# Kernel optimization log

Hardware: AMD Instinct MI355X
Metric: run time of the kernel (lower is better)

## Reference

```python
import jax, jax.numpy as jnp
import numpy as np

B, T, N = 64, 128, 64   # batch, win_size, input_size (= node_num)
H, E, K, CS = 64, 128, 7, 8  # hidden_size, embed_size, kernel_size, control_size
NEG_SLOPE = 0.2


def _p(key, shape, scale=0.05):
    return scale * jax.random.normal(key, shape, dtype=jnp.float32)


def setup_inputs() -> dict:
    key = jax.random.key(0)
    ks = jax.random.split(key, 32)
    inp = {
        "x": jax.random.normal(ks[0], (B, T, N), dtype=jnp.float32),
        "y": jax.random.normal(ks[1], (B, T, CS), dtype=jnp.float32),
        # Conv1d(N -> N, kernel K)
        "conv_w": _p(ks[2], (N, N, K)),
        "conv_b": _p(ks[3], (N,)),
        # rnn_enc GRU: input N -> hidden H
        "We_ih": _p(ks[4], (3 * H, N)), "We_hh": _p(ks[5], (3 * H, H)),
        "be_ih": _p(ks[6], (3 * H,)), "be_hh": _p(ks[7], (3 * H,)),
        # MP_GAT linears
        "Ww": _p(ks[8], (E, 2 * T)), "bw": _p(ks[9], (E,)),
        "Wa": _p(ks[10], (1, E)), "ba": _p(ks[11], (1,)),
        # encoder GRU: input H+N -> H
        "Wm_ih": _p(ks[12], (3 * H, H + N)), "Wm_hh": _p(ks[13], (3 * H, H)),
        "bm_ih": _p(ks[14], (3 * H,)), "bm_hh": _p(ks[15], (3 * H,)),
        # rnn_dec GRU: input H -> H
        "Wd_ih": _p(ks[16], (3 * H, H)), "Wd_hh": _p(ks[17], (3 * H, H)),
        "bd_ih": _p(ks[18], (3 * H,)), "bd_hh": _p(ks[19], (3 * H,)),
        # fc_dec: H -> N
        "W_dec": _p(ks[20], (N, H)), "b_dec": _p(ks[21], (N,)),
        # fc_pred: Linear(H,N), ReLU, Linear(N,N)
        "W_p1": _p(ks[22], (N, H)), "b_p1": _p(ks[23], (N,)),
        "W_p2": _p(ks[24], (N, N)), "b_p2": _p(ks[25], (N,)),
    }
    return inp


def gru_seq(x_seq, Wih, Whh, bih, bhh):
    """torch nn.GRU (batch_first, h0=0). x_seq: [B,T,in] -> [B,T,H]."""
    gi = jnp.einsum('bti,gi->btg', x_seq, Wih) + bih  # [B,T,3H] (precompute input proj)
    h0 = jnp.zeros((x_seq.shape[0], Whh.shape[1]), x_seq.dtype)

    def step(h, gi_t):
        gh = h @ Whh.T + bhh
        i_r, i_z, i_n = jnp.split(gi_t, 3, axis=-1)
        h_r, h_z, h_n = jnp.split(gh, 3, axis=-1)
        r = jax.nn.sigmoid(i_r + h_r)
        z = jax.nn.sigmoid(i_z + h_z)
        n = jnp.tanh(i_n + r * h_n)
        h_new = (1.0 - z) * n + z * h
        return h_new, h_new

    _, hs = jax.lax.scan(step, h0, jnp.swapaxes(gi, 0, 1))
    return jnp.swapaxes(hs, 0, 1)


def _forward(x, y, conv_w, conv_b, We_ih, We_hh, be_ih, be_hh, Ww, bw, Wa, ba,
             Wm_ih, Wm_hh, bm_ih, bm_hh, Wd_ih, Wd_hh, bd_ih, bd_hh,
             W_dec, b_dec, W_p1, b_p1, W_p2, b_p2):
    # ---- CNN: pad 'same' + Conv1d + SELU. x: [B,T,N] -> channels first [B,N,T]
    pad = (K - 1) // 2
    xc = jnp.swapaxes(x, 1, 2)
    c = jax.lax.conv_general_dilated(xc, conv_w, (1,), [(pad, pad)],
                                     dimension_numbers=('NCH', 'OIH', 'NCH'))
    c = jax.nn.selu(c + conv_b[None, :, None])  # [B,N,T]
    c_btn = jnp.swapaxes(c, 1, 2)               # [B,T,N]

    # ---- rnn_enc GRU over time
    h_out = gru_seq(c_btn, We_ih, We_hh, be_ih, be_hh)  # [B,T,H]

    # ---- MP_GAT on c (v: [B, node, seq] = [B,N,T])
    v = c
    vi = jnp.broadcast_to(v[:, :, None, :], (B, N, N, T))
    vj = jnp.broadcast_to(v[:, None, :, :], (B, N, N, T))
    v_cat = jnp.concatenate([vi, vj], axis=-1)          # [B,N,N,2T]
    x_w = jax.nn.leaky_relu(jnp.einsum('bijt,et->bije', v_cat, Ww) + bw, NEG_SLOPE)
    e = (jnp.einsum('bije,oe->bijo', x_w, Wa) + ba)[..., 0]  # [B,N,N]
    attention = jax.nn.softmax(e, axis=2)
    # dropout is identity in eval mode
    h_mp = jax.nn.sigmoid(jnp.einsum('bij,bjt->bit', attention, v))  # [B,N,T]
    h_mp = jnp.swapaxes(h_mp, 1, 2)                      # [B,T,N]

    # ---- encoder / decoder GRUs (dropout = identity in eval)
    h_cat = jnp.concatenate([h_out, h_mp], axis=2)       # [B,T,H+N]
    h_enc = gru_seq(h_cat, Wm_ih, Wm_hh, bm_ih, bm_hh)
    h_dec = gru_seq(h_enc, Wd_ih, Wd_hh, bd_ih, bd_hh)

    recon = h_dec @ W_dec.T + b_dec                      # [B,T,N]
    p = jax.nn.relu(h_dec[:, 0, :] @ W_p1.T + b_p1)
    pred = p @ W_p2.T + b_p2                             # [B,N]
    return recon, pred


def reference(x, y, conv_w, conv_b, We_ih, We_hh, be_ih, be_hh, Ww, bw, Wa, ba,
              Wm_ih, Wm_hh, bm_ih, bm_hh, Wd_ih, Wd_hh, bd_ih, bd_hh,
              W_dec, b_dec, W_p1, b_p1, W_p2, b_p2):
    return _forward(x, y, conv_w, conv_b, We_ih, We_hh, be_ih, be_hh, Ww, bw, Wa, ba,
                    Wm_ih, Wm_hh, bm_ih, bm_hh, Wd_ih, Wd_hh, bd_ih, bd_hh,
                    W_dec, b_dec, W_p1, b_p1, W_p2, b_p2)
```

## Files before the change

kernel.cpp:

```cpp
#include <hip/hip_runtime.h>
#include <math.h>

#define BB 64
#define TT 128
#define NN 64
#define HH 64
#define EE 128
#define KK 7
#define GG 192

typedef _Float16 half2_t __attribute__((ext_vector_type(2)));

__device__ __forceinline__ float sigmoidf_(float x){ return 1.f/(1.f+expf(-x)); }
__device__ __forceinline__ float fsig_(float x){
  return __builtin_amdgcn_rcpf(1.f + __builtin_amdgcn_exp2f(-1.44269504f * x));
}
__device__ __forceinline__ float ftanh_(float x){
  return fmaf(-2.f, __builtin_amdgcn_rcpf(1.f + __builtin_amdgcn_exp2f(2.88539008f * x)), 1.f);
}

#define PIPE_BARRIER() asm volatile("s_waitcnt lgkmcnt(0)\ns_barrier" ::: "memory")

__device__ __forceinline__ void loadrow_(float* d, const float* src){
  const float4* p = (const float4*)src;
  #pragma unroll
  for (int i = 0; i < 16; ++i) {
    float4 v = p[i];
    d[4*i] = v.x; d[4*i+1] = v.y; d[4*i+2] = v.z; d[4*i+3] = v.w;
  }
}
__device__ __forceinline__ void loadroww_(half2_t* d, const float* src){
  const float4* p = (const float4*)src;
  #pragma unroll
  for (int i = 0; i < 16; ++i) {
    float4 v = p[i];
    d[2*i]   = half2_t{(_Float16)v.x, (_Float16)v.y};
    d[2*i+1] = half2_t{(_Float16)v.z, (_Float16)v.w};
  }
}
__device__ __forceinline__ void load_h16_(const _Float16* hs, half2_t* hp){
  const float4* s4 = (const float4*)hs;
  #pragma unroll
  for (int j = 0; j < 8; ++j) {
    float4 v = s4[j];
    const half2_t* q = (const half2_t*)&v;
    hp[4*j] = q[0]; hp[4*j+1] = q[1]; hp[4*j+2] = q[2]; hp[4*j+3] = q[3];
  }
}
__device__ __forceinline__ void mvdot3_(const half2_t* hp, const half2_t* w0,
                                        const half2_t* w1, const half2_t* w2,
                                        float& a0, float& a1, float& a2){
  #pragma unroll
  for (int i = 0; i < 32; ++i) {
    a0 = __builtin_amdgcn_fdot2(hp[i], w0[i], a0, false);
    a1 = __builtin_amdgcn_fdot2(hp[i], w1[i], a1, false);
    a2 = __builtin_amdgcn_fdot2(hp[i], w2[i], a2, false);
  }
}

__global__ void conv_selu_kernel(const float* __restrict__ x, const float* __restrict__ w,
                                 const float* __restrict__ bias,
                                 float* __restrict__ c_nt, float* __restrict__ c_btn) {
  const int og = blockIdx.x, b = blockIdx.y, t = threadIdx.x;
  const int o0 = og * 8;
  __shared__ __align__(16) float xs[NN][TT + 1];
  __shared__ __align__(16) float ws[NN * KK][8];
  for (int idx = t; idx < TT * NN; idx += 128) {
    int tt = idx >> 6, nn = idx & 63;
    xs[nn][tt] = x[(size_t)(b * TT + tt) * NN + nn];
  }
  for (int idx = t; idx < NN * KK * 8; idx += 128) {
    int oo = idx & 7, ik = idx >> 3;
    ws[ik][oo] = w[(size_t)(o0 + oo) * (NN * KK) + ik];
  }
  __syncthreads();
  float acc[8];
  #pragma unroll
  for (int oo = 0; oo < 8; ++oo) acc[oo] = bias[o0 + oo];
  for (int i = 0; i < NN; ++i) {
    #pragma unroll
    for (int k = 0; k < KK; ++k) {
      int tt = t + k - 3;
      if (tt >= 0 && tt < TT) {
        float xv = xs[i][tt];
        const float* wp = &ws[i * KK + k][0];
        float4 w0 = *(const float4*)wp;
        float4 w1 = *(const float4*)(wp + 4);
        acc[0] += xv * w0.x; acc[1] += xv * w0.y; acc[2] += xv * w0.z; acc[3] += xv * w0.w;
        acc[4] += xv * w1.x; acc[5] += xv * w1.y; acc[6] += xv * w1.z; acc[7] += xv * w1.w;
      }
    }
  }
  const float alpha = 1.6732632423543772f, scale = 1.0507009873554805f;
  #pragma unroll
  for (int oo = 0; oo < 8; ++oo) {
    float a = acc[oo];
    float r = a > 0.f ? scale * a : scale * alpha * expm1f(a);
    int o = o0 + oo;
    c_nt[((size_t)b * NN + o) * TT + t] = r;
    c_btn[((size_t)b * TT + t) * NN + o] = r;
  }
}

__global__ void s12_kernel(const float* __restrict__ c_nt, const float* __restrict__ Ww,
                           float* __restrict__ s1, float* __restrict__ s2) {
  const int m0 = blockIdx.x * 16, col = threadIdx.x;
  __shared__ __align__(16) float ins[16][TT];
  for (int idx = col; idx < 16 * TT; idx += 128) {
    int r = idx >> 7, k = idx & 127;
    ins[r][k] = c_nt[(size_t)(m0 + r) * TT + k];
  }
  __syncthreads();
  const float* w1 = Ww + (size_t)col * (2 * TT);
  const float* w2 = w1 + TT;
  float acc1[16], acc2[16];
  #pragma unroll
  for (int r = 0; r < 16; ++r) { acc1[r] = 0.f; acc2[r] = 0.f; }
  #pragma unroll 2
  for (int k = 0; k < TT; k += 4) {
    float4 wv1 = *(const float4*)(w1 + k);
    float4 wv2 = *(const float4*)(w2 + k);
    #pragma unroll
    for (int r = 0; r < 16; ++r) {
      float4 iv = *(const float4*)&ins[r][k];
      acc1[r] += iv.x * wv1.x + iv.y * wv1.y + iv.z * wv1.z + iv.w * wv1.w;
      acc2[r] += iv.x * wv2.x + iv.y * wv2.y + iv.z * wv2.z + iv.w * wv2.w;
    }
  }
  #pragma unroll
  for (int r = 0; r < 16; ++r) {
    s1[(size_t)(m0 + r) * EE + col] = acc1[r];
    s2[(size_t)(m0 + r) * EE + col] = acc2[r];
  }
}

__global__ void gat_kernel(const float* __restrict__ s1, const float* __restrict__ s2,
                           const float* __restrict__ bw, const float* __restrict__ Wa,
                           const float* __restrict__ ba, const float* __restrict__ c_nt,
                           float* __restrict__ hmp) {
  const int i = blockIdx.x, b = blockIdx.y, tid = threadIdx.x;
  __shared__ float s2s[NN][EE + 1];
  __shared__ float s1b[EE], was[EE], att[NN];
  for (int idx = tid; idx < NN * EE; idx += 128) {
    int r = idx >> 7, e = idx & 127;
    s2s[r][e] = s2[((size_t)b * NN + r) * EE + e];
  }
  s1b[tid] = s1[((size_t)b * NN + i) * EE + tid] + bw[tid];
  was[tid] = Wa[tid];
  __syncthreads();
  if (tid < NN) {
    float acc = 0.f;
    #pragma unroll 8
    for (int e = 0; e < EE; ++e) {
      float wv = s1b[e] + s2s[tid][e];
      wv = wv > 0.f ? wv : 0.2f * wv;
      acc += was[e] * wv;
    }
    float ej = acc + ba[0];
    float mx = ej;
    for (int off = 32; off >= 1; off >>= 1) mx = fmaxf(mx, __shfl_xor(mx, off));
    float ex = expf(ej - mx);
    float sm = ex;
    for (int off = 32; off >= 1; off >>= 1) sm += __shfl_xor(sm, off);
    att[tid] = ex / sm;
  }
  __syncthreads();
  float acc = 0.f;
  #pragma unroll 8
  for (int j = 0; j < NN; ++j) acc += att[j] * c_nt[((size_t)b * NN + j) * TT + tid];
  hmp[((size_t)b * TT + tid) * NN + i] = sigmoidf_(acc);
}

__global__ __launch_bounds__(512, 1)
void fused_chain8(const float* __restrict__ c_btn, const float* __restrict__ hmp,
                  const float* __restrict__ We_ih, const float* __restrict__ be_ih,
                  const float* __restrict__ We_hh, const float* __restrict__ be_hh,
                  const float* __restrict__ Wm_ih, const float* __restrict__ bm_ih,
                  const float* __restrict__ Wm_hh, const float* __restrict__ bm_hh,
                  const float* __restrict__ Wd_ih, const float* __restrict__ bd_ih,
                  const float* __restrict__ Wd_hh, const float* __restrict__ bd_hh,
                  const float* __restrict__ W_dec, const float* __restrict__ b_dec,
                  const float* __restrict__ W_p1, const float* __restrict__ b_p1,
                  const float* __restrict__ W_p2, const float* __restrict__ b_p2,
                  float* __restrict__ recon, float* __restrict__ pred) {
  const int b = blockIdx.x, tid = threadIdx.x, wid = tid >> 6, g = tid & 63;
  __shared__ __align__(16) _Float16 cbuf[2][HH], mbuf[2][HH];
  __shared__ __align__(16) _Float16 h1h[2][HH], h2h[2][HH], h3h[2][HH];
  __shared__ __align__(16) float h3f[2][HH];
  __shared__ __align__(16) float q1[2][GG], q2a[2][GG], q2b[2][GG], q3[2][GG];
  __shared__ __align__(16) float h0s[HH], ps[HH];

  half2_t wa[32], wb[32], wc[32];
  float wdec[64];
  float b0 = 0.f, b1 = 0.f, b2 = 0.f;
  float e0 = 0.f, e1 = 0.f, e2 = 0.f;
  if (wid == 0) {
    loadroww_(wa, We_hh + (size_t)g * HH);
    loadroww_(wb, We_hh + (size_t)(g + 64) * HH);
    loadroww_(wc, We_hh + (size_t)(g + 128) * HH);
    b0 = be_hh[g]; b1 = be_hh[64 + g]; b2 = be_hh[128 + g];
  } else if (wid == 1) {
    loadroww_(wa, Wm_hh + (size_t)g * HH);
    loadroww_(wb, Wm_hh + (size_t)(g + 64) * HH);
    loadroww_(wc, Wm_hh + (size_t)(g + 128) * HH);
    b0 = bm_hh[g]; b1 = bm_hh[64 + g]; b2 = bm_hh[128 + g];
  } else if (wid == 2) {
    loadroww_(wa, Wd_hh + (size_t)g * HH);
    loadroww_(wb, Wd_hh + (size_t)(g + 64) * HH);
    loadroww_(wc, Wd_hh + (size_t)(g + 128) * HH);
    b0 = bd_hh[g]; b1 = bd_hh[64 + g]; b2 = bd_hh[128 + g];
    e0 = bd_ih[g]; e1 = bd_ih[64 + g]; e2 = bd_ih[128 + g];
  } else if (wid == 3) {
    loadrow_(wdec, W_dec + (size_t)g * HH);
    b0 = b_dec[g];
  } else if (wid == 4) {
    loadroww_(wa, Wm_ih + (size_t)g * 128);
    loadroww_(wb, Wm_ih + (size_t)(g + 64) * 128);
    loadroww_(wc, Wm_ih + (size_t)(g + 128) * 128);
  } else if (wid == 5) {
    loadroww_(wa, Wd_ih + (size_t)g * HH);
    loadroww_(wb, Wd_ih + (size_t)(g + 64) * HH);
    loadroww_(wc, Wd_ih + (size_t)(g + 128) * HH);
  } else if (wid == 6) {
    loadroww_(wa, We_ih + (size_t)g * HH);
    loadroww_(wb, We_ih + (size_t)(g + 64) * HH);
    loadroww_(wc, We_ih + (size_t)(g + 128) * HH);
    b0 = be_ih[g]; b1 = be_ih[64 + g]; b2 = be_ih[128 + g];
  } else {
    loadroww_(wa, Wm_ih + (size_t)g * 128 + 64);
    loadroww_(wb, Wm_ih + (size_t)(g + 64) * 128 + 64);
    loadroww_(wc, Wm_ih + (size_t)(g + 128) * 128 + 64);
    b0 = bm_ih[g]; b1 = bm_ih[64 + g]; b2 = bm_ih[128 + g];
  }

  if (wid == 0) {
    h1h[0][g] = (_Float16)0.f; h1h[1][g] = (_Float16)0.f;
    h2h[0][g] = (_Float16)0.f; h2h[1][g] = (_Float16)0.f;
    h3h[0][g] = (_Float16)0.f; h3h[1][g] = (_Float16)0.f;
  }
  const float* cb = c_btn + (size_t)b * TT * NN + g;
  const float* hm = hmp   + (size_t)b * TT * NN + g;
  float pf0 = 0.f, pf1 = 0.f;
  if (wid == 6) {
    cbuf[0][g] = (_Float16)cb[0]; cbuf[1][g] = (_Float16)cb[NN];
    pf0 = cb[2 * NN]; pf1 = cb[3 * NN];
  }
  if (wid == 7) {
    mbuf[0][g] = (_Float16)hm[0]; mbuf[1][g] = (_Float16)hm[NN];
    pf0 = hm[2 * NN]; pf1 = hm[3 * NN];
  }
  if (wid <= 2) __builtin_amdgcn_s_setprio(1);
  __syncthreads();

  float hown = 0.f;
  for (int ph = 0; ph < TT + 6; ++ph) {
    const int pw = ph & 1, pr = pw ^ 1;
    if (wid == 6) {
      int t = ph;
      if (t < TT) {
        half2_t hp[32]; load_h16_(&cbuf[pw][0], hp);
        if (t + 2 < TT) cbuf[pw][g] = (_Float16)(pw ? pf1 : pf0);
        float a0 = b0, a1 = b1, a2 = b2;
        if (t + 4 < TT) { float nv = cb[(size_t)(t + 4) * NN]; if (pw) pf1 = nv; else pf0 = nv; }
        mvdot3_(hp, wa, wb, wc, a0, a1, a2);
        q1[pw][g] = a0; q1[pw][64 + g] = a1; q1[pw][128 + g] = a2;
      }
    } else if (wid == 0) {
      int t = ph - 1;
      if (t >= 0 && t < TT) {
        half2_t hp[32]; load_h16_(&h1h[pr][0], hp);
        float a0 = b0, a1 = b1, a2 = b2;
        mvdot3_(hp, wa, wb, wc, a0, a1, a2);
        float r = fsig_(q1[pr][g] + a0), z = fsig_(q1[pr][64 + g] + a1);
        float n = ftanh_(q1[pr][128 + g] + r * a2);
        hown = fmaf(z, hown - n, n);
        h1h[pw][g] = (_Float16)hown;
      }
    } else if (wid == 4) {
      int t = ph - 2;
      if (t >= 0 && t < TT) {
        half2_t hp[32]; load_h16_(&h1h[pr][0], hp);
        float a0 = 0.f, a1 = 0.f, a2 = 0.f;
        mvdot3_(hp, wa, wb, wc, a0, a1, a2);
        q2a[pw][g] = a0; q2a[pw][64 + g] = a1; q2a[pw][128 + g] = a2;
      }
    } else if (wid == 7) {
      int t = ph - 2;
      if (t >= 0 && t < TT) {
        half2_t hp[32]; load_h16_(&mbuf[pw][0], hp);
        if (t + 2 < TT) mbuf[pw][g] = (_Float16)(pw ? pf1 : pf0);
        float a0 = b0, a1 = b1, a2 = b2;
        if (t + 4 < TT) { float nv = hm[(size_t)(t + 4) * NN]; if (pw) pf1 = nv; else pf0 = nv; }
        mvdot3_(hp, wa, wb, wc, a0, a1, a2);
        q2b[pw][g] = a0; q2b[pw][64 + g] = a1; q2b[pw][128 + g] = a2;
      }
    } else if (wid == 1) {
      int t = ph - 3;
      if (t >= 0 && t < TT) {
        half2_t hp[32]; load_h16_(&h2h[pr][0], hp);
        float a0 = b0, a1 = b1, a2 = b2;
        mvdot3_(hp, wa, wb, wc, a0, a1, a2);
        float gr = q2a[pr][g] + q2b[pr][g];
        float gz = q2a[pr][64 + g] + q2b[pr][64 + g];
        float gn = q2a[pr][128 + g] + q2b[pr][128 + g];
        float r = fsig_(gr + a0), z = fsig_(gz + a1), n = ftanh_(gn + r * a2);
        hown = fmaf(z, hown - n, n);
        h2h[pw][g] = (_Float16)hown;
      }
    } else if (wid == 5) {
      int t = ph - 4;
      if (t >= 0 && t < TT) {
        half2_t hp[32]; load_h16_(&h2h[pr][0], hp);
        float a0 = 0.f, a1 = 0.f, a2 = 0.f;
        mvdot3_(hp, wa, wb, wc, a0, a1, a2);
        q3[pw][g] = a0; q3[pw][64 + g] = a1; q3[pw][128 + g] = a2;
      }
    } else if (wid == 2) {
      int t = ph - 5;
      if (t >= 0 && t < TT) {
        half2_t hp[32]; load_h16_(&h3h[pr][0], hp);
        float a0 = b0, a1 = b1, a2 = b2;
        mvdot3_(hp, wa, wb, wc, a0, a1, a2);
        float r = fsig_(q3[pr][g] + e0 + a0), z = fsig_(q3[pr][64 + g] + e1 + a1);
        float n = ftanh_(q3[pr][128 + g] + e2 + r * a2);
        hown = fmaf(z, hown - n, n);
        h3h[pw][g] = (_Float16)hown;
        h3f[pw][g] = hown;
        if (t == 0) h0s[g] = hown;
      }
    } else {
      int t = ph - 6;
      if (t >= 0) {
        const float4* h4 = (const float4*)&h3f[pr][0];
        float a0 = b0, a1 = 0.f;
        #pragma unroll
        for (int i = 0; i < 8; ++i) {
          float4 hv = h4[2 * i], hw = h4[2 * i + 1];
          a0 = fmaf(hv.x, wdec[8*i],   fmaf(hv.y, wdec[8*i+1], fmaf(hv.z, wdec[8*i+2], fmaf(hv.w, wdec[8*i+3], a0))));
          a1 = fmaf(hw.x, wdec[8*i+4], fmaf(hw.y, wdec[8*i+5], fmaf(hw.z, wdec[8*i+6], fmaf(hw.w, wdec[8*i+7], a1))));
        }
        recon[((size_t)b * TT + t) * NN + g] = a0 + a1;
      }
    }
    PIPE_BARRIER();
  }

  if (wid == 0) {
    float w1r[64]; loadrow_(w1r, W_p1 + (size_t)g * HH);
    const float4* h4 = (const float4*)&h0s[0];
    float a = b_p1[g];
    #pragma unroll
    for (int i = 0; i < 16; ++i) {
      float4 hv = h4[i];
      a = fmaf(hv.x, w1r[4*i], fmaf(hv.y, w1r[4*i+1], fmaf(hv.z, w1r[4*i+2], fmaf(hv.w, w1r[4*i+3], a))));
    }
    ps[g] = fmaxf(a, 0.f);
    asm volatile("s_waitcnt lgkmcnt(0)" ::: "memory");
    float w2r[64]; loadrow_(w2r, W_p2 + (size_t)g * HH);
    const float4* p4 = (const float4*)&ps[0];
    float c2 = b_p2[g];
    #pragma unroll
    for (int i = 0; i < 16; ++i) {
      float4 pv = p4[i];
      c2 = fmaf(pv.x, w2r[4*i], fmaf(pv.y, w2r[4*i+1], fmaf(pv.z, w2r[4*i+2], fmaf(pv.w, w2r[4*i+3], c2))));
    }
    pred[(size_t)b * NN + g] = c2;
  }
}

extern "C" void kernel_launch(void* const* d_in, const int* in_sizes, int n_in,
                              void* d_out, int out_size, void* d_ws, size_t ws_size,
                              hipStream_t stream) {
  const float* x      = (const float*)d_in[0];
  const float* conv_w = (const float*)d_in[2];
  const float* conv_b = (const float*)d_in[3];
  const float* We_ih  = (const float*)d_in[4];
  const float* We_hh  = (const float*)d_in[5];
  const float* be_ih  = (const float*)d_in[6];
  const float* be_hh  = (const float*)d_in[7];
  const float* Ww     = (const float*)d_in[8];
  const float* bw     = (const float*)d_in[9];
  const float* Wa     = (const float*)d_in[10];
  const float* ba     = (const float*)d_in[11];
  const float* Wm_ih  = (const float*)d_in[12];
  const float* Wm_hh  = (const float*)d_in[13];
  const float* bm_ih  = (const float*)d_in[14];
  const float* bm_hh  = (const float*)d_in[15];
  const float* Wd_ih  = (const float*)d_in[16];
  const float* Wd_hh  = (const float*)d_in[17];
  const float* bd_ih  = (const float*)d_in[18];
  const float* bd_hh  = (const float*)d_in[19];
  const float* W_dec  = (const float*)d_in[20];
  const float* b_dec  = (const float*)d_in[21];
  const float* W_p1   = (const float*)d_in[22];
  const float* b_p1   = (const float*)d_in[23];
  const float* W_p2   = (const float*)d_in[24];
  const float* b_p2   = (const float*)d_in[25];
  float* out = (float*)d_out;

  float* wsf   = (float*)d_ws;
  float* c_nt  = wsf;
  float* c_btn = c_nt  + 524288;
  float* s1    = c_btn + 524288;
  float* s2    = s1    + 524288;
  float* hmp   = s2    + 524288;

  conv_selu_kernel<<<dim3(8, BB), 128, 0, stream>>>(x, conv_w, conv_b, c_nt, c_btn);
  s12_kernel<<<BB * NN / 16, 128, 0, stream>>>(c_nt, Ww, s1, s2);
  gat_kernel<<<dim3(NN, BB), 128, 0, stream>>>(s1, s2, bw, Wa, ba, c_nt, hmp);
  fused_chain8<<<BB, 512, 0, stream>>>(c_btn, hmp,
                                       We_ih, be_ih, We_hh, be_hh,
                                       Wm_ih, bm_ih, Wm_hh, bm_hh,
                                       Wd_ih, bd_ih, Wd_hh, bd_hh,
                                       W_dec, b_dec, W_p1, b_p1, W_p2, b_p2,
                                       out, out + BB * TT * NN);
}
```

Baseline: 206.0 us.

## Restructure GRU chain pipeline to 4 waves and batch GAT rows per block

The fused recurrent chain drops from 8 to 4 waves per block. Each wave now computes both the input and hidden projections of one GRU layer, so the pipeline depth shrinks from 6 stages to 4 with fewer barrier phases and fewer shared-memory staging buffers. The GAT kernel processes 16 attention rows per block with c_nt cached in shared memory, which cuts redundant s2 and c_nt reloads, and it uses exp2 in the softmax. The cost is more work per wave on the serial critical path (six dot-product accumulators instead of three) and higher register pressure.

```diff
diff --git a/kernel.cpp b/kernel.cpp
--- a/kernel.cpp
+++ b/kernel.cpp
@@ -20,6 +20,7 @@
 }
 
 #define PIPE_BARRIER() asm volatile("s_waitcnt lgkmcnt(0)\ns_barrier" ::: "memory")
+#define LGKM0() asm volatile("s_waitcnt lgkmcnt(0)" ::: "memory")
 
 __device__ __forceinline__ void loadrow_(float* d, const float* src){
   const float4* p = (const float4*)src;
@@ -36,25 +37,6 @@
     float4 v = p[i];
     d[2*i]   = half2_t{(_Float16)v.x, (_Float16)v.y};
     d[2*i+1] = half2_t{(_Float16)v.z, (_Float16)v.w};
-  }
-}
-__device__ __forceinline__ void load_h16_(const _Float16* hs, half2_t* hp){
-  const float4* s4 = (const float4*)hs;
-  #pragma unroll
-  for (int j = 0; j < 8; ++j) {
-    float4 v = s4[j];
-    const half2_t* q = (const half2_t*)&v;
-    hp[4*j] = q[0]; hp[4*j+1] = q[1]; hp[4*j+2] = q[2]; hp[4*j+3] = q[3];
-  }
-}
-__device__ __forceinline__ void mvdot3_(const half2_t* hp, const half2_t* w0,
-                                        const half2_t* w1, const half2_t* w2,
-                                        float& a0, float& a1, float& a2){
-  #pragma unroll
-  for (int i = 0; i < 32; ++i) {
-    a0 = __builtin_amdgcn_fdot2(hp[i], w0[i], a0, false);
-    a1 = __builtin_amdgcn_fdot2(hp[i], w1[i], a1, false);
-    a2 = __builtin_amdgcn_fdot2(hp[i], w2[i], a2, false);
   }
 }
 
@@ -138,41 +120,58 @@
                            const float* __restrict__ bw, const float* __restrict__ Wa,
                            const float* __restrict__ ba, const float* __restrict__ c_nt,
                            float* __restrict__ hmp) {
-  const int i = blockIdx.x, b = blockIdx.y, tid = threadIdx.x;
+  const int it = blockIdx.x, b = blockIdx.y, tid = threadIdx.x;
+  const int i0 = it * 16;
   __shared__ float s2s[NN][EE + 1];
-  __shared__ float s1b[EE], was[EE], att[NN];
-  for (int idx = tid; idx < NN * EE; idx += 128) {
+  __shared__ float s1b[16][EE];
+  __shared__ float cs[NN][TT + 1];
+  __shared__ float was[EE];
+  __shared__ float att[16][NN];
+  for (int idx = tid; idx < NN * EE; idx += 256) {
+    int j = idx >> 7, e = idx & 127;
+    s2s[j][e] = s2[((size_t)b * NN + j) * EE + e] + bw[e];
+  }
+  for (int idx = tid; idx < 16 * EE; idx += 256) {
     int r = idx >> 7, e = idx & 127;
-    s2s[r][e] = s2[((size_t)b * NN + r) * EE + e];
-  }
-  s1b[tid] = s1[((size_t)b * NN + i) * EE + tid] + bw[tid];
-  was[tid] = Wa[tid];
+    s1b[r][e] = s1[((size_t)b * NN + i0 + r) * EE + e];
+  }
+  for (int idx = tid; idx < NN * TT; idx += 256) {
+    int j = idx >> 7, t = idx & 127;
+    cs[j][t] = c_nt[((size_t)b * NN + j) * TT + t];
+  }
+  if (tid < EE) was[tid] = Wa[tid];
   __syncthreads();
-  if (tid < NN) {
+  const int wv = tid >> 6, j = tid & 63;
+  #pragma unroll
+  for (int pass = 0; pass < 4; ++pass) {
+    const int il = pass * 4 + wv;
     float acc = 0.f;
     #pragma unroll 8
     for (int e = 0; e < EE; ++e) {
-      float wv = s1b[e] + s2s[tid][e];
-      wv = wv > 0.f ? wv : 0.2f * wv;
-      acc += was[e] * wv;
+      float v = s1b[il][e] + s2s[j][e];
+      v = v > 0.f ? v : 0.2f * v;
+      acc += was[e] * v;
     }
     float ej = acc + ba[0];
     float mx = ej;
     for (int off = 32; off >= 1; off >>= 1) mx = fmaxf(mx, __shfl_xor(mx, off));
-    float ex = expf(ej - mx);
+    float ex = __builtin_amdgcn_exp2f(1.44269504f * (ej - mx));
     float sm = ex;
     for (int off = 32; off >= 1; off >>= 1) sm += __shfl_xor(sm, off);
-    att[tid] = ex / sm;
+    att[il][j] = ex / sm;
   }
   __syncthreads();
-  float acc = 0.f;
-  #pragma unroll 8
-  for (int j = 0; j < NN; ++j) acc += att[j] * c_nt[((size_t)b * NN + j) * TT + tid];
-  hmp[((size_t)b * TT + tid) * NN + i] = sigmoidf_(acc);
-}
-
-__global__ __launch_bounds__(512, 1)
-void fused_chain8(const float* __restrict__ c_btn, const float* __restrict__ hmp,
+  for (int o = tid; o < 16 * TT; o += 256) {
+    int il = o >> 7, t = o & 127;
+    float acc = 0.f;
+    #pragma unroll 8
+    for (int jj = 0; jj < NN; ++jj) acc += att[il][jj] * cs[jj][t];
+    hmp[((size_t)b * TT + t) * NN + i0 + il] = sigmoidf_(acc);
+  }
+}
+
+__global__ __launch_bounds__(256, 1)
+void fused_chain4(const float* __restrict__ c_btn, const float* __restrict__ hmp,
                   const float* __restrict__ We_ih, const float* __restrict__ be_ih,
                   const float* __restrict__ We_hh, const float* __restrict__ be_hh,
                   const float* __restrict__ Wm_ih, const float* __restrict__ bm_ih,
@@ -184,168 +183,191 @@
                   const float* __restrict__ W_p2, const float* __restrict__ b_p2,
                   float* __restrict__ recon, float* __restrict__ pred) {
   const int b = blockIdx.x, tid = threadIdx.x, wid = tid >> 6, g = tid & 63;
-  __shared__ __align__(16) _Float16 cbuf[2][HH], mbuf[2][HH];
-  __shared__ __align__(16) _Float16 h1h[2][HH], h2h[2][HH], h3h[2][HH];
-  __shared__ __align__(16) float h3f[2][HH];
-  __shared__ __align__(16) float q1[2][GG], q2a[2][GG], q2b[2][GG], q3[2][GG];
+  __shared__ __align__(16) _Float16 cbuf[HH], mbuf[HH], h3h[HH];
+  __shared__ __align__(16) _Float16 h1h[2][HH], h2h[2][HH];
+  __shared__ __align__(16) float q2[2][GG], h3f[2][HH];
   __shared__ __align__(16) float h0s[HH], ps[HH];
 
-  half2_t wa[32], wb[32], wc[32];
+  half2_t wxa[32], wxb[32], wxc[32];
+  half2_t wya[32], wyb[32], wyc[32];
   float wdec[64];
-  float b0 = 0.f, b1 = 0.f, b2 = 0.f;
-  float e0 = 0.f, e1 = 0.f, e2 = 0.f;
+  float b0 = 0.f, b1 = 0.f, b2 = 0.f, e0 = 0.f, e1 = 0.f, e2 = 0.f, bdc = 0.f;
   if (wid == 0) {
-    loadroww_(wa, We_hh + (size_t)g * HH);
-    loadroww_(wb, We_hh + (size_t)(g + 64) * HH);
-    loadroww_(wc, We_hh + (size_t)(g + 128) * HH);
-    b0 = be_hh[g]; b1 = be_hh[64 + g]; b2 = be_hh[128 + g];
+    loadroww_(wxa, We_ih + (size_t)g * HH);
+    loadroww_(wxb, We_ih + (size_t)(g + 64) * HH);
+    loadroww_(wxc, We_ih + (size_t)(g + 128) * HH);
+    loadroww_(wya, We_hh + (size_t)g * HH);
+    loadroww_(wyb, We_hh + (size_t)(g + 64) * HH);
+    loadroww_(wyc, We_hh + (size_t)(g + 128) * HH);
+    b0 = be_ih[g]; b1 = be_ih[64 + g]; b2 = be_ih[128 + g];
+    e0 = be_hh[g]; e1 = be_hh[64 + g]; e2 = be_hh[128 + g];
   } else if (wid == 1) {
-    loadroww_(wa, Wm_hh + (size_t)g * HH);
-    loadroww_(wb, Wm_hh + (size_t)(g + 64) * HH);
-    loadroww_(wc, Wm_hh + (size_t)(g + 128) * HH);
+    loadroww_(wxa, Wm_ih + (size_t)g * 128);
+    loadroww_(wxb, Wm_ih + (size_t)(g + 64) * 128);
+    loadroww_(wxc, Wm_ih + (size_t)(g + 128) * 128);
+    loadroww_(wya, Wm_ih + (size_t)g * 128 + 64);
+    loadroww_(wyb, Wm_ih + (size_t)(g + 64) * 128 + 64);
+    loadroww_(wyc, Wm_ih + (size_t)(g + 128) * 128 + 64);
+    b0 = bm_ih[g]; b1 = bm_ih[64 + g]; b2 = bm_ih[128 + g];
+  } else if (wid == 2) {
+    loadroww_(wxa, Wm_hh + (size_t)g * HH);
+    loadroww_(wxb, Wm_hh + (size_t)(g + 64) * HH);
+    loadroww_(wxc, Wm_hh + (size_t)(g + 128) * HH);
+    loadrow_(wdec, W_dec + (size_t)g * HH);
     b0 = bm_hh[g]; b1 = bm_hh[64 + g]; b2 = bm_hh[128 + g];
-  } else if (wid == 2) {
-    loadroww_(wa, Wd_hh + (size_t)g * HH);
-    loadroww_(wb, Wd_hh + (size_t)(g + 64) * HH);
-    loadroww_(wc, Wd_hh + (size_t)(g + 128) * HH);
-    b0 = bd_hh[g]; b1 = bd_hh[64 + g]; b2 = bd_hh[128 + g];
-    e0 = bd_ih[g]; e1 = bd_ih[64 + g]; e2 = bd_ih[128 + g];
-  } else if (wid == 3) {
-    loadrow_(wdec, W_dec + (size_t)g * HH);
-    b0 = b_dec[g];
-  } else if (wid == 4) {
-    loadroww_(wa, Wm_ih + (size_t)g * 128);
-    loadroww_(wb, Wm_ih + (size_t)(g + 64) * 128);
-    loadroww_(wc, Wm_ih + (size_t)(g + 128) * 128);
-  } else if (wid == 5) {
-    loadroww_(wa, Wd_ih + (size_t)g * HH);
-    loadroww_(wb, Wd_ih + (size_t)(g + 64) * HH);
-    loadroww_(wc, Wd_ih + (size_t)(g + 128) * HH);
-  } else if (wid == 6) {
-    loadroww_(wa, We_ih + (size_t)g * HH);
-    loadroww_(wb, We_ih + (size_t)(g + 64) * HH);
-    loadroww_(wc, We_ih + (size_t)(g + 128) * HH);
-    b0 = be_ih[g]; b1 = be_ih[64 + g]; b2 = be_ih[128 + g];
+    bdc = b_dec[g];
   } else {
-    loadroww_(wa, Wm_ih + (size_t)g * 128 + 64);
-    loadroww_(wb, Wm_ih + (size_t)(g + 64) * 128 + 64);
-    loadroww_(wc, Wm_ih + (size_t)(g + 128) * 128 + 64);
-    b0 = bm_ih[g]; b1 = bm_ih[64 + g]; b2 = bm_ih[128 + g];
-  }
-
+    loadroww_(wxa, Wd_ih + (size_t)g * HH);
+    loadroww_(wxb, Wd_ih + (size_t)(g + 64) * HH);
+    loadroww_(wxc, Wd_ih + (size_t)(g + 128) * HH);
+    loadroww_(wya, Wd_hh + (size_t)g * HH);
+    loadroww_(wyb, Wd_hh + (size_t)(g + 64) * HH);
+    loadroww_(wyc, Wd_hh + (size_t)(g + 128) * HH);
+    b0 = bd_ih[g]; b1 = bd_ih[64 + g]; b2 = bd_ih[128 + g];
+    e0 = bd_hh[g]; e1 = bd_hh[64 + g]; e2 = bd_hh[128 + g];
+  }
   if (wid == 0) {
     h1h[0][g] = (_Float16)0.f; h1h[1][g] = (_Float16)0.f;
     h2h[0][g] = (_Float16)0.f; h2h[1][g] = (_Float16)0.f;
-    h3h[0][g] = (_Float16)0.f; h3h[1][g] = (_Float16)0.f;
+    h3h[g]    = (_Float16)0.f;
   }
   const float* cb = c_btn + (size_t)b * TT * NN + g;
   const float* hm = hmp   + (size_t)b * TT * NN + g;
-  float pf0 = 0.f, pf1 = 0.f;
-  if (wid == 6) {
-    cbuf[0][g] = (_Float16)cb[0]; cbuf[1][g] = (_Float16)cb[NN];
-    pf0 = cb[2 * NN]; pf1 = cb[3 * NN];
-  }
-  if (wid == 7) {
-    mbuf[0][g] = (_Float16)hm[0]; mbuf[1][g] = (_Float16)hm[NN];
-    pf0 = hm[2 * NN]; pf1 = hm[3 * NN];
-  }
-  if (wid <= 2) __builtin_amdgcn_s_setprio(1);
+  float cc = 0.f, cn = 0.f;
+  if (wid == 0) { cc = cb[0]; cn = cb[NN]; }
+  if (wid == 1) { cc = hm[0]; cn = hm[NN]; }
+  float hown = 0.f;
   __syncthreads();
 
-  float hown = 0.f;
-  for (int ph = 0; ph < TT + 6; ++ph) {
-    const int pw = ph & 1, pr = pw ^ 1;
-    if (wid == 6) {
-      int t = ph;
+  for (int p = 0; p < TT + 4; ++p) {
+    const int pw = p & 1, pr = pw ^ 1;
+    if (wid == 0) {
+      int t = p;
       if (t < TT) {
-        half2_t hp[32]; load_h16_(&cbuf[pw][0], hp);
-        if (t + 2 < TT) cbuf[pw][g] = (_Float16)(pw ? pf1 : pf0);
-        float a0 = b0, a1 = b1, a2 = b2;
-        if (t + 4 < TT) { float nv = cb[(size_t)(t + 4) * NN]; if (pw) pf1 = nv; else pf0 = nv; }
-        mvdot3_(hp, wa, wb, wc, a0, a1, a2);
-        q1[pw][g] = a0; q1[pw][64 + g] = a1; q1[pw][128 + g] = a2;
-      }
-    } else if (wid == 0) {
-      int t = ph - 1;
-      if (t >= 0 && t < TT) {
-        half2_t hp[32]; load_h16_(&h1h[pr][0], hp);
-        float a0 = b0, a1 = b1, a2 = b2;
-        mvdot3_(hp, wa, wb, wc, a0, a1, a2);
-        float r = fsig_(q1[pr][g] + a0), z = fsig_(q1[pr][64 + g] + a1);
-        float n = ftanh_(q1[pr][128 + g] + r * a2);
+        cbuf[g] = (_Float16)cc;
+        float cl = 0.f;
+        if (t + 2 < TT) cl = cb[(size_t)(t + 2) * NN];
+        LGKM0();
+        float a0 = b0, a1 = b1, a2 = b2, r0 = e0, r1 = e1, r2 = e2;
+        const float4* c4 = (const float4*)&cbuf[0];
+        const float4* h4 = (const float4*)&h1h[pr][0];
+        #pragma unroll
+        for (int ch = 0; ch < 8; ++ch) {
+          float4 cv = c4[ch], hv = h4[ch];
+          const half2_t* cq = (const half2_t*)&cv;
+          const half2_t* hq = (const half2_t*)&hv;
+          #pragma unroll
+          for (int k = 0; k < 4; ++k) {
+            int i = 4 * ch + k;
+            a0 = __builtin_amdgcn_fdot2(cq[k], wxa[i], a0, false);
+            a1 = __builtin_amdgcn_fdot2(cq[k], wxb[i], a1, false);
+            a2 = __builtin_amdgcn_fdot2(cq[k], wxc[i], a2, false);
+            r0 = __builtin_amdgcn_fdot2(hq[k], wya[i], r0, false);
+            r1 = __builtin_amdgcn_fdot2(hq[k], wyb[i], r1, false);
+            r2 = __builtin_amdgcn_fdot2(hq[k], wyc[i], r2, false);
+          }
+        }
+        float r = fsig_(a0 + r0), z = fsig_(a1 + r1), n = ftanh_(a2 + r * r2);
         hown = fmaf(z, hown - n, n);
         h1h[pw][g] = (_Float16)hown;
-      }
-    } else if (wid == 4) {
-      int t = ph - 2;
+        cc = cn; cn = cl;
+      }
+    } else if (wid == 1) {
+      int t = p - 1;
       if (t >= 0 && t < TT) {
-        half2_t hp[32]; load_h16_(&h1h[pr][0], hp);
-        float a0 = 0.f, a1 = 0.f, a2 = 0.f;
-        mvdot3_(hp, wa, wb, wc, a0, a1, a2);
-        q2a[pw][g] = a0; q2a[pw][64 + g] = a1; q2a[pw][128 + g] = a2;
-      }
-    } else if (wid == 7) {
-      int t = ph - 2;
+        mbuf[g] = (_Float16)cc;
+        float cl = 0.f;
+        if (t + 2 < TT) cl = hm[(size_t)(t + 2) * NN];
+        LGKM0();
+        float a0 = b0, a1 = b1, a2 = b2, r0 = 0.f, r1 = 0.f, r2 = 0.f;
+        const float4* h4 = (const float4*)&h1h[pr][0];
+        const float4* m4 = (const float4*)&mbuf[0];
+        #pragma unroll
+        for (int ch = 0; ch < 8; ++ch) {
+          float4 hv = h4[ch], mv = m4[ch];
+          const half2_t* hq = (const half2_t*)&hv;
+          const half2_t* mq = (const half2_t*)&mv;
+          #pragma unroll
+          for (int k = 0; k < 4; ++k) {
+            int i = 4 * ch + k;
+            a0 = __builtin_amdgcn_fdot2(hq[k], wxa[i], a0, false);
+            a1 = __builtin_amdgcn_fdot2(hq[k], wxb[i], a1, false);
+            a2 = __builtin_amdgcn_fdot2(hq[k], wxc[i], a2, false);
+            r0 = __builtin_amdgcn_fdot2(mq[k], wya[i], r0, false);
+            r1 = __builtin_amdgcn_fdot2(mq[k], wyb[i], r1, false);
+            r2 = __builtin_amdgcn_fdot2(mq[k], wyc[i], r2, false);
+          }
+        }
+        q2[pw][g] = a0 + r0; q2[pw][64 + g] = a1 + r1; q2[pw][128 + g] = a2 + r2;
+        cc = cn; cn = cl;
+      }
+    } else if (wid == 2) {
+      int t = p - 2;
       if (t >= 0 && t < TT) {
-        half2_t hp[32]; load_h16_(&mbuf[pw][0], hp);
-        if (t + 2 < TT) mbuf[pw][g] = (_Float16)(pw ? pf1 : pf0);
         float a0 = b0, a1 = b1, a2 = b2;
-        if (t + 4 < TT) { float nv = hm[(size_t)(t + 4) * NN]; if (pw) pf1 = nv; else pf0 = nv; }
-        mvdot3_(hp, wa, wb, wc, a0, a1, a2);
-        q2b[pw][g] = a0; q2b[pw][64 + g] = a1; q2b[pw][128 + g] = a2;
-      }
-    } else if (wid == 1) {
-      int t = ph - 3;
-      if (t >= 0 && t < TT) {
-        half2_t hp[32]; load_h16_(&h2h[pr][0], hp);
-        float a0 = b0, a1 = b1, a2 = b2;
-        mvdot3_(hp, wa, wb, wc, a0, a1, a2);
-        float gr = q2a[pr][g] + q2b[pr][g];
-        float gz = q2a[pr][64 + g] + q2b[pr][64 + g];
-        float gn = q2a[pr][128 + g] + q2b[pr][128 + g];
-        float r = fsig_(gr + a0), z = fsig_(gz + a1), n = ftanh_(gn + r * a2);
+        const float4* h4 = (const float4*)&h2h[pr][0];
+        #pragma unroll
+        for (int ch = 0; ch < 8; ++ch) {
+          float4 hv = h4[ch];
+          const half2_t* hq = (const half2_t*)&hv;
+          #pragma unroll
+          for (int k = 0; k < 4; ++k) {
+            int i = 4 * ch + k;
+            a0 = __builtin_amdgcn_fdot2(hq[k], wxa[i], a0, false);
+            a1 = __builtin_amdgcn_fdot2(hq[k], wxb[i], a1, false);
+            a2 = __builtin_amdgcn_fdot2(hq[k], wxc[i], a2, false);
+          }
+        }
+        float r = fsig_(q2[pr][g] + a0), z = fsig_(q2[pr][64 + g] + a1);
+        float n = ftanh_(q2[pr][128 + g] + r * a2);
         hown = fmaf(z, hown - n, n);
         h2h[pw][g] = (_Float16)hown;
       }
-    } else if (wid == 5) {
-      int t = ph - 4;
-      if (t >= 0 && t < TT) {
-        half2_t hp[32]; load_h16_(&h2h[pr][0], hp);
-        float a0 = 0.f, a1 = 0.f, a2 = 0.f;
-        mvdot3_(hp, wa, wb, wc, a0, a1, a2);
-        q3[pw][g] = a0; q3[pw][64 + g] = a1; q3[pw][128 + g] = a2;
-      }
-    } else if (wid == 2) {
-      int t = ph - 5;
-      if (t >= 0 && t < TT) {
-        half2_t hp[32]; load_h16_(&h3h[pr][0], hp);
-        float a0 = b0, a1 = b1, a2 = b2;
-        mvdot3_(hp, wa, wb, wc, a0, a1, a2);
-        float r = fsig_(q3[pr][g] + e0 + a0), z = fsig_(q3[pr][64 + g] + e1 + a1);
-        float n = ftanh_(q3[pr][128 + g] + e2 + r * a2);
-        hown = fmaf(z, hown - n, n);
-        h3h[pw][g] = (_Float16)hown;
-        h3f[pw][g] = hown;
-        if (t == 0) h0s[g] = hown;
-      }
-    } else {
-      int t = ph - 6;
-      if (t >= 0) {
+      int t4 = p - 4;
+      if (t4 >= 0) {
         const float4* h4 = (const float4*)&h3f[pr][0];
-        float a0 = b0, a1 = 0.f;
+        float a0 = bdc, a1 = 0.f;
         #pragma unroll
         for (int i = 0; i < 8; ++i) {
           float4 hv = h4[2 * i], hw = h4[2 * i + 1];
           a0 = fmaf(hv.x, wdec[8*i],   fmaf(hv.y, wdec[8*i+1], fmaf(hv.z, wdec[8*i+2], fmaf(hv.w, wdec[8*i+3], a0))));
           a1 = fmaf(hw.x, wdec[8*i+4], fmaf(hw.y, wdec[8*i+5], fmaf(hw.z, wdec[8*i+6], fmaf(hw.w, wdec[8*i+7], a1))));
         }
-        recon[((size_t)b * TT + t) * NN + g] = a0 + a1;
+        recon[((size_t)b * TT + t4) * NN + g] = a0 + a1;
+      }
+    } else {
+      int t = p - 3;
+      if (t >= 0 && t < TT) {
+        float a0 = b0, a1 = b1, a2 = b2, r0 = e0, r1 = e1, r2 = e2;
+        const float4* h4 = (const float4*)&h2h[pr][0];
+        const float4* o4 = (const float4*)&h3h[0];
+        #pragma unroll
+        for (int ch = 0; ch < 8; ++ch) {
+          float4 hv = h4[ch], ov = o4[ch];
+          const half2_t* hq = (const half2_t*)&hv;
+          const half2_t* oq = (const half2_t*)&ov;
+          #pragma unroll
+          for (int k = 0; k < 4; ++k) {
+            int i = 4 * ch + k;
+            a0 = __builtin_amdgcn_fdot2(hq[k], wxa[i], a0, false);
+            a1 = __builtin_amdgcn_fdot2(hq[k], wxb[i], a1, false);
+            a2 = __builtin_amdgcn_fdot2(hq[k], wxc[i], a2, false);
+            r0 = __builtin_amdgcn_fdot2(oq[k], wya[i], r0, false);
+            r1 = __builtin_amdgcn_fdot2(oq[k], wyb[i], r1, false);
+            r2 = __builtin_amdgcn_fdot2(oq[k], wyc[i], r2, false);
+          }
+        }
+        float r = fsig_(a0 + r0), z = fsig_(a1 + r1), n = ftanh_(a2 + r * r2);
+        hown = fmaf(z, hown - n, n);
+        h3h[g] = (_Float16)hown;
+        h3f[pw][g] = hown;
+        if (t == 0) h0s[g] = hown;
       }
     }
     PIPE_BARRIER();
   }
 
-  if (wid == 0) {
+  if (wid == 2) {
     float w1r[64]; loadrow_(w1r, W_p1 + (size_t)g * HH);
     const float4* h4 = (const float4*)&h0s[0];
     float a = b_p1[g];
@@ -355,7 +377,7 @@
       a = fmaf(hv.x, w1r[4*i], fmaf(hv.y, w1r[4*i+1], fmaf(hv.z, w1r[4*i+2], fmaf(hv.w, w1r[4*i+3], a))));
     }
     ps[g] = fmaxf(a, 0.f);
-    asm volatile("s_waitcnt lgkmcnt(0)" ::: "memory");
+    LGKM0();
     float w2r[64]; loadrow_(w2r, W_p2 + (size_t)g * HH);
     const float4* p4 = (const float4*)&ps[0];
     float c2 = b_p2[g];
@@ -407,8 +429,8 @@
 
   conv_selu_kernel<<<dim3(8, BB), 128, 0, stream>>>(x, conv_w, conv_b, c_nt, c_btn);
   s12_kernel<<<BB * NN / 16, 128, 0, stream>>>(c_nt, Ww, s1, s2);
-  gat_kernel<<<dim3(NN, BB), 128, 0, stream>>>(s1, s2, bw, Wa, ba, c_nt, hmp);
-  fused_chain8<<<BB, 512, 0, stream>>>(c_btn, hmp,
+  gat_kernel<<<dim3(4, BB), 256, 0, stream>>>(s1, s2, bw, Wa, ba, c_nt, hmp);
+  fused_chain4<<<BB, 256, 0, stream>>>(c_btn, hmp,
                                        We_ih, be_ih, We_hh, be_hh,
                                        Wm_ih, bm_ih, Wm_hh, bm_hh,
                                        Wd_ih, bd_ih, Wd_hh, bd_hh,
```

Result: slower. 212.0 us (+2.9%).

## Fuse s12 projection into conv kernel and batch GAT rows per block

Applied to the files above, without the earlier changes.

Merges the S1/S2 linear projection into the conv+SELU kernel, so the freshly computed conv outputs are consumed from shared memory instead of being re-read from global memory by a separate launch. The GAT kernel now handles 16 query nodes per 256-thread block instead of one node per 128-thread block. This amortizes the loads of s2 and c_nt over 16 rows and stages c_nt in shared memory. It also folds the bias into s2 and uses a hardware exp2 in the softmax. In exchange the GAT launch has far fewer blocks (256) with much higher shared memory use per block, which lowers parallelism.

```diff
diff --git a/kernel.cpp b/kernel.cpp
--- a/kernel.cpp
+++ b/kernel.cpp
@@ -20,6 +20,7 @@
 }
 
 #define PIPE_BARRIER() asm volatile("s_waitcnt lgkmcnt(0)\ns_barrier" ::: "memory")
+#define LGKM0() asm volatile("s_waitcnt lgkmcnt(0)" ::: "memory")
 
 __device__ __forceinline__ void loadrow_(float* d, const float* src){
   const float4* p = (const float4*)src;
@@ -58,13 +59,15 @@
   }
 }
 
-__global__ void conv_selu_kernel(const float* __restrict__ x, const float* __restrict__ w,
-                                 const float* __restrict__ bias,
-                                 float* __restrict__ c_nt, float* __restrict__ c_btn) {
+__global__ void conv_s12_kernel(const float* __restrict__ x, const float* __restrict__ w,
+                                const float* __restrict__ bias, const float* __restrict__ Ww,
+                                float* __restrict__ c_nt, float* __restrict__ c_btn,
+                                float* __restrict__ s1, float* __restrict__ s2) {
   const int og = blockIdx.x, b = blockIdx.y, t = threadIdx.x;
   const int o0 = og * 8;
   __shared__ __align__(16) float xs[NN][TT + 1];
   __shared__ __align__(16) float ws[NN * KK][8];
+  __shared__ __align__(16) float cs[8][TT];
   for (int idx = t; idx < TT * NN; idx += 128) {
     int tt = idx >> 6, nn = idx & 63;
     xs[nn][tt] = x[(size_t)(b * TT + tt) * NN + nn];
@@ -99,38 +102,29 @@
     int o = o0 + oo;
     c_nt[((size_t)b * NN + o) * TT + t] = r;
     c_btn[((size_t)b * TT + t) * NN + o] = r;
-  }
-}
-
-__global__ void s12_kernel(const float* __restrict__ c_nt, const float* __restrict__ Ww,
-                           float* __restrict__ s1, float* __restrict__ s2) {
-  const int m0 = blockIdx.x * 16, col = threadIdx.x;
-  __shared__ __align__(16) float ins[16][TT];
-  for (int idx = col; idx < 16 * TT; idx += 128) {
-    int r = idx >> 7, k = idx & 127;
-    ins[r][k] = c_nt[(size_t)(m0 + r) * TT + k];
+    cs[oo][t] = r;
   }
   __syncthreads();
-  const float* w1 = Ww + (size_t)col * (2 * TT);
+  const float* w1 = Ww + (size_t)t * (2 * TT);
   const float* w2 = w1 + TT;
-  float acc1[16], acc2[16];
-  #pragma unroll
-  for (int r = 0; r < 16; ++r) { acc1[r] = 0.f; acc2[r] = 0.f; }
+  float a1[8], a2l[8];
+  #pragma unroll
+  for (int r = 0; r < 8; ++r) { a1[r] = 0.f; a2l[r] = 0.f; }
   #pragma unroll 2
   for (int k = 0; k < TT; k += 4) {
     float4 wv1 = *(const float4*)(w1 + k);
     float4 wv2 = *(const float4*)(w2 + k);
     #pragma unroll
-    for (int r = 0; r < 16; ++r) {
-      float4 iv = *(const float4*)&ins[r][k];
-      acc1[r] += iv.x * wv1.x + iv.y * wv1.y + iv.z * wv1.z + iv.w * wv1.w;
-      acc2[r] += iv.x * wv2.x + iv.y * wv2.y + iv.z * wv2.z + iv.w * wv2.w;
-    }
-  }
-  #pragma unroll
-  for (int r = 0; r < 16; ++r) {
-    s1[(size_t)(m0 + r) * EE + col] = acc1[r];
-    s2[(size_t)(m0 + r) * EE + col] = acc2[r];
+    for (int r = 0; r < 8; ++r) {
+      float4 cv = *(const float4*)&cs[r][k];
+      a1[r]  += cv.x * wv1.x + cv.y * wv1.y + cv.z * wv1.z + cv.w * wv1.w;
+      a2l[r] += cv.x * wv2.x + cv.y * wv2.y + cv.z * wv2.z + cv.w * wv2.w;
+    }
+  }
+  #pragma unroll
+  for (int r = 0; r < 8; ++r) {
+    s1[((size_t)b * NN + o0 + r) * EE + t] = a1[r];
+    s2[((size_t)b * NN + o0 + r) * EE + t] = a2l[r];
   }
 }
 
@@ -138,37 +132,54 @@
                            const float* __restrict__ bw, const float* __restrict__ Wa,
                            const float* __restrict__ ba, const float* __restrict__ c_nt,
                            float* __restrict__ hmp) {
-  const int i = blockIdx.x, b = blockIdx.y, tid = threadIdx.x;
+  const int it = blockIdx.x, b = blockIdx.y, tid = threadIdx.x;
+  const int i0 = it * 16;
   __shared__ float s2s[NN][EE + 1];
-  __shared__ float s1b[EE], was[EE], att[NN];
-  for (int idx = tid; idx < NN * EE; idx += 128) {
+  __shared__ float s1b[16][EE];
+  __shared__ float cs[NN][TT + 1];
+  __shared__ float was[EE];
+  __shared__ float att[16][NN];
+  for (int idx = tid; idx < NN * EE; idx += 256) {
+    int j = idx >> 7, e = idx & 127;
+    s2s[j][e] = s2[((size_t)b * NN + j) * EE + e] + bw[e];
+  }
+  for (int idx = tid; idx < 16 * EE; idx += 256) {
     int r = idx >> 7, e = idx & 127;
-    s2s[r][e] = s2[((size_t)b * NN + r) * EE + e];
-  }
-  s1b[tid] = s1[((size_t)b * NN + i) * EE + tid] + bw[tid];
-  was[tid] = Wa[tid];
+    s1b[r][e] = s1[((size_t)b * NN + i0 + r) * EE + e];
+  }
+  for (int idx = tid; idx < NN * TT; idx += 256) {
+    int j = idx >> 7, t = idx & 127;
+    cs[j][t] = c_nt[((size_t)b * NN + j) * TT + t];
+  }
+  if (tid < EE) was[tid] = Wa[tid];
   __syncthreads();
-  if (tid < NN) {
+  const int wv = tid >> 6, j = tid & 63;
+  #pragma unroll
+  for (int pass = 0; pass < 4; ++pass) {
+    const int il = pass * 4 + wv;
     float acc = 0.f;
     #pragma unroll 8
     for (int e = 0; e < EE; ++e) {
-      float wv = s1b[e] + s2s[tid][e];
-      wv = wv > 0.f ? wv : 0.2f * wv;
-      acc += was[e] * wv;
+      float v = s1b[il][e] + s2s[j][e];
+      v = v > 0.f ? v : 0.2f * v;
+      acc += was[e] * v;
     }
     float ej = acc + ba[0];
     float mx = ej;
     for (int off = 32; off >= 1; off >>= 1) mx = fmaxf(mx, __shfl_xor(mx, off));
-    float ex = expf(ej - mx);
+    float ex = __builtin_amdgcn_exp2f(1.44269504f * (ej - mx));
     float sm = ex;
     for (int off = 32; off >= 1; off >>= 1) sm += __shfl_xor(sm, off);
-    att[tid] = ex / sm;
+    att[il][j] = ex / sm;
   }
   __syncthreads();
-  float acc = 0.f;
-  #pragma unroll 8
-  for (int j = 0; j < NN; ++j) acc += att[j] * c_nt[((size_t)b * NN + j) * TT + tid];
-  hmp[((size_t)b * TT + tid) * NN + i] = sigmoidf_(acc);
+  for (int o = tid; o < 16 * TT; o += 256) {
+    int il = o >> 7, t = o & 127;
+    float acc = 0.f;
+    #pragma unroll 8
+    for (int jj = 0; jj < NN; ++jj) acc += att[il][jj] * cs[jj][t];
+    hmp[((size_t)b * TT + t) * NN + i0 + il] = sigmoidf_(acc);
+  }
 }
 
 __global__ __launch_bounds__(512, 1)
@@ -355,7 +366,7 @@
       a = fmaf(hv.x, w1r[4*i], fmaf(hv.y, w1r[4*i+1], fmaf(hv.z, w1r[4*i+2], fmaf(hv.w, w1r[4*i+3], a))));
     }
     ps[g] = fmaxf(a, 0.f);
-    asm volatile("s_waitcnt lgkmcnt(0)" ::: "memory");
+    LGKM0();
     float w2r[64]; loadrow_(w2r, W_p2 + (size_t)g * HH);
     const float4* p4 = (const float4*)&ps[0];
     float c2 = b_p2[g];
@@ -405,9 +416,9 @@
   float* s2    = s1    + 524288;
   float* hmp   = s2    + 524288;
 
-  conv_selu_kernel<<<dim3(8, BB), 128, 0, stream>>>(x, conv_w, conv_b, c_nt, c_btn);
-  s12_kernel<<<BB * NN / 16, 128, 0, stream>>>(c_nt, Ww, s1, s2);
-  gat_kernel<<<dim3(NN, BB), 128, 0, stream>>>(s1, s2, bw, Wa, ba, c_nt, hmp);
+  conv_s12_kernel<<<dim3(8, BB), 128, 0, stream>>>(x, conv_w, conv_b, Ww,
+                                                   c_nt, c_btn, s1, s2);
+  gat_kernel<<<dim3(4, BB), 256, 0, stream>>>(s1, s2, bw, Wa, ba, c_nt, hmp);
   fused_chain8<<<BB, 512, 0, stream>>>(c_btn, hmp,
                                        We_ih, be_ih, We_hh, be_hh,
                                        Wm_ih, bm_ih, Wm_hh, bm_hh,
```

Measured after the change: 182.6 us. 11.3% less time.
